# Optimization experiments

Hardware: AMD Instinct MI355X
Metric: run time of the kernel (lower is better)

The kernel has to match this reference:

```python
import jax, jax.numpy as jnp
import numpy as np

GROUPS = 32
EPS = 1e-6


def group_norm(x, gamma, beta):
    # x: [b, c, d, h, w]
    b, c, d, h, w = x.shape
    xg = x.reshape(b, GROUPS, c // GROUPS, d, h, w)
    mean = xg.mean(axis=(2, 3, 4, 5), keepdims=True)
    var = xg.var(axis=(2, 3, 4, 5), keepdims=True)
    xn = ((xg - mean) * jax.lax.rsqrt(var + EPS)).reshape(b, c, d, h, w)
    return xn * gamma[None, :, None, None, None] + beta[None, :, None, None, None]


def conv1x1(x, w, bias):
    # 1x1x1 Conv3d == channel matmul. x: [b,c,d,h,w], w: [out,in]
    return jnp.einsum('bcdhw,oc->bodhw', x, w) + bias[None, :, None, None, None]


def setup_inputs() -> dict:
    key = jax.random.key(0)
    ks = jax.random.split(key, 6)
    C = 256
    x = jax.random.normal(ks[0], (4, C, 16, 16, 16), dtype=jnp.float32)
    s = 1.0 / np.sqrt(C)
    return {
        'x': x,
        'gn_gamma': jnp.ones((C,), jnp.float32),
        'gn_beta': jnp.zeros((C,), jnp.float32),
        'wq': jax.random.normal(ks[1], (C, C), jnp.float32) * s,
        'bq': jnp.zeros((C,), jnp.float32),
        'wk': jax.random.normal(ks[2], (C, C), jnp.float32) * s,
        'bk': jnp.zeros((C,), jnp.float32),
        'wv': jax.random.normal(ks[3], (C, C), jnp.float32) * s,
        'bv': jnp.zeros((C,), jnp.float32),
        'wo': jax.random.normal(ks[4], (C, C), jnp.float32) * s,
        'bo': jnp.zeros((C,), jnp.float32),
    }


def reference(x, gn_gamma, gn_beta, wq, bq, wk, bk, wv, bv, wo, bo):
    b, c, d, h, w = x.shape
    n = d * h * w
    hn = group_norm(x, gn_gamma, gn_beta)
    q = conv1x1(hn, wq, bq).reshape(b, c, n)  # [b,c,n]
    k = conv1x1(hn, wk, bk).reshape(b, c, n)
    v = conv1x1(hn, wv, bv).reshape(b, c, n)
    # NOTE: no 1/sqrt(c) scaling, faithful to source
    scores = jnp.einsum('bci,bcj->bij', q, k)          # [b,n,n]
    attn = jax.nn.softmax(scores, axis=-1)
    out = jnp.einsum('bij,bcj->bci', attn, v)           # [b,c,n]
    out = out.reshape(b, c, d, h, w)
    out = conv1x1(out, wo, bo)
    return x + out
```

## Files before the change

### kernel.cpp

```cpp
#include <hip/hip_runtime.h>
#include <hip/hip_bf16.h>

#define C_ 256
#define N_ 4096
#define B_ 4
#define NG_ 32
#define CPG_ 8
#define SPLITS 2
#define JT_PER (N_ / 32 / SPLITS)

typedef _Float16 f16;
typedef __attribute__((ext_vector_type(8))) _Float16 f16v8;
typedef __attribute__((ext_vector_type(2))) __fp16 fp16v2;
typedef __attribute__((ext_vector_type(4))) float f32x4;

__device__ __forceinline__ f16v8 ldh(const f16* p) {
    return *reinterpret_cast<const f16v8*>(p);
}
__device__ __forceinline__ f32x4 mfma16(f16v8 a, f16v8 b, f32x4 c) {
    return __builtin_amdgcn_mfma_f32_16x16x32_f16(a, b, c, 0, 0, 0);
}
__device__ __forceinline__ unsigned int pkh(float a, float b) {
    fp16v2 t = __builtin_amdgcn_cvt_pkrtz(a, b);
    return __builtin_bit_cast(unsigned int, t);
}

__global__ __launch_bounds__(256) void conv_w_kernel(
    const float* __restrict__ wq, const float* __restrict__ wk,
    const float* __restrict__ wv, const float* __restrict__ wo,
    f16* __restrict__ wq16, f16* __restrict__ wk16,
    f16* __restrict__ wv16, f16* __restrict__ wo16)
{
    int idx = blockIdx.x * 256 + threadIdx.x;
    wq16[idx] = (f16)wq[idx];
    wk16[idx] = (f16)wk[idx];
    wv16[idx] = (f16)wv[idx];
    wo16[idx] = (f16)wo[idx];
}

__global__ __launch_bounds__(256) void gn_kernel(
    const float* __restrict__ x, const float* __restrict__ gamma,
    const float* __restrict__ beta, f16* __restrict__ hn)
{
    int b = blockIdx.x >> 5, g = blockIdx.x & 31;
    const float* xp = x + (size_t)(b * C_ + g * CPG_) * N_;
    int tid = threadIdx.x;
    float s = 0.f, s2 = 0.f;
    for (int idx = tid; idx < CPG_ * N_; idx += 256) {
        float v = xp[idx];
        s += v; s2 += v * v;
    }
    #pragma unroll
    for (int off = 32; off > 0; off >>= 1) {
        s  += __shfl_down(s, off);
        s2 += __shfl_down(s2, off);
    }
    __shared__ float rs[4], rs2[4], stat[2];
    if ((tid & 63) == 0) { rs[tid >> 6] = s; rs2[tid >> 6] = s2; }
    __syncthreads();
    if (tid == 0) {
        float S  = rs[0] + rs[1] + rs[2] + rs[3];
        float S2 = rs2[0] + rs2[1] + rs2[2] + rs2[3];
        float mean = S / (float)(CPG_ * N_);
        float var  = S2 / (float)(CPG_ * N_) - mean * mean;
        stat[0] = mean;
        stat[1] = rsqrtf(var + 1e-6f);
    }
    __syncthreads();
    float mean = stat[0], rstd = stat[1];
    float ga[CPG_], be[CPG_];
    #pragma unroll
    for (int cc = 0; cc < CPG_; cc++) {
        ga[cc] = gamma[g * CPG_ + cc] * rstd;
        be[cc] = beta[g * CPG_ + cc];
    }
    for (int i = tid; i < N_; i += 256) {
        f16v8 H;
        #pragma unroll
        for (int cc = 0; cc < CPG_; cc++)
            H[cc] = (f16)((xp[(size_t)cc * N_ + i] - mean) * ga[cc] + be[cc]);
        *reinterpret_cast<f16v8*>(hn + (size_t)(b * N_ + i) * C_ + g * CPG_) = H;
    }
}

__global__ __launch_bounds__(256) void proj_qk_kernel(
    const f16* __restrict__ hn, const f16* __restrict__ wq16,
    const f16* __restrict__ wk16, const float* __restrict__ bq,
    const float* __restrict__ bk, f16* __restrict__ qo, f16* __restrict__ ko)
{
    int it = blockIdx.x, b = blockIdx.y, which = blockIdx.z;
    const f16* wgt = which ? wk16 : wq16;
    const float* bias = which ? bk : bq;
    f16* outp = which ? ko : qo;
    int tid = threadIdx.x, w = tid >> 6, l = tid & 63;
    int l15 = l & 15, lhi = l >> 4;
    int i0 = it * 64 + w * 16;
    size_t arow = (size_t)(b * N_ + i0 + l15) * C_ + lhi * 8;
    f16v8 af[8];
    #pragma unroll
    for (int kk = 0; kk < 8; kk++) af[kk] = ldh(hn + arow + kk * 32);
    for (int oc = 0; oc < 16; oc++) {
        f32x4 acc = {0.f, 0.f, 0.f, 0.f};
        size_t wrow = (size_t)(oc * 16 + l15) * C_ + lhi * 8;
        #pragma unroll
        for (int kk = 0; kk < 8; kk++)
            acc = mfma16(af[kk], ldh(wgt + wrow + kk * 32), acc);
        float bia = bias[oc * 16 + l15];
        #pragma unroll
        for (int r = 0; r < 4; r++)
            outp[(size_t)(b * N_ + i0 + lhi * 4 + r) * C_ + oc * 16 + l15] =
                (f16)(acc[r] + bia);
    }
}

__global__ __launch_bounds__(256) void proj_v_kernel(
    const f16* __restrict__ hn, const f16* __restrict__ wv16,
    const float* __restrict__ bv, f16* __restrict__ vT)
{
    int it = blockIdx.x, b = blockIdx.y;
    int tid = threadIdx.x, w = tid >> 6, l = tid & 63;
    int l15 = l & 15, lhi = l >> 4;
    int o0 = w * 64, i0 = it * 64;
    f32x4 acc[4][4];
    #pragma unroll
    for (int mc = 0; mc < 4; mc++)
        #pragma unroll
        for (int nc = 0; nc < 4; nc++) acc[mc][nc] = (f32x4){0.f, 0.f, 0.f, 0.f};
    for (int kk = 0; kk < 8; kk++) {
        f16v8 af[4], bfv[4];
        #pragma unroll
        for (int mc = 0; mc < 4; mc++)
            af[mc] = ldh(wv16 + (size_t)(o0 + mc * 16 + l15) * C_ + kk * 32 + lhi * 8);
        #pragma unroll
        for (int nc = 0; nc < 4; nc++)
            bfv[nc] = ldh(hn + (size_t)(b * N_ + i0 + nc * 16 + l15) * C_ + kk * 32 + lhi * 8);
        #pragma unroll
        for (int mc = 0; mc < 4; mc++)
            #pragma unroll
            for (int nc = 0; nc < 4; nc++)
                acc[mc][nc] = mfma16(af[mc], bfv[nc], acc[mc][nc]);
    }
    #pragma unroll
    for (int mc = 0; mc < 4; mc++) {
        float bia[4];
        #pragma unroll
        for (int r = 0; r < 4; r++) bia[r] = bv[o0 + mc * 16 + lhi * 4 + r];
        #pragma unroll
        for (int nc = 0; nc < 4; nc++)
            #pragma unroll
            for (int r = 0; r < 4; r++) {
                int o = o0 + mc * 16 + lhi * 4 + r;
                int i = i0 + nc * 16 + l15;
                vT[(size_t)(b * C_ + o) * N_ + i] = (f16)(acc[mc][nc][r] + bia[r]);
            }
    }
}

__device__ __forceinline__ void stage_k(const f16* kbase, f16* dst, int j0,
                                        int w, int l) {
    #pragma unroll
    for (int rd = 0; rd < 4; rd++) {
        int cb = (rd * 4 + w) * 64;
        int mc = cb + l;
        int row = mc >> 5;
        int xoff = ((mc & 31) << 4) ^ ((row & 7) << 4);
        const f16* gsrc = kbase + (size_t)(j0 + row) * C_ + (xoff >> 1);
        __builtin_amdgcn_global_load_lds(
            (const __attribute__((address_space(1))) void*)gsrc,
            (__attribute__((address_space(3))) void*)(dst + (size_t)cb * 8),
            16, 0, 0);
    }
}
__device__ __forceinline__ void stage_v(const f16* vbase, f16* dst, int j0,
                                        int w, int l) {
    int tid = w * 64 + l;
    int colu = ((l & 3) ^ ((l >> 3) & 3)) * 8;
    #pragma unroll
    for (int s = 0; s < 4; s++) {
        int cb = s * 256 + w * 64;
        const f16* gsrc = vbase + (size_t)(s * 64 + (tid >> 2)) * N_ + j0 + colu;
        __builtin_amdgcn_global_load_lds(
            (const __attribute__((address_space(1))) void*)gsrc,
            (__attribute__((address_space(3))) void*)(dst + (size_t)cb * 8),
            16, 0, 0);
    }
}

__global__ __launch_bounds__(256, 2) void flash_split_kernel(
    const f16* __restrict__ q, const f16* __restrict__ k,
    const f16* __restrict__ vT,
    f16* __restrict__ o0p, f16* __restrict__ o1p,
    float2* __restrict__ stats)
{
    int bi = blockIdx.x;
    int g = bi & 7;
    int it = bi >> 3;
    int b = g >> 1, split = g & 1;
    int tid = threadIdx.x, w = tid >> 6, l = tid & 63;
    int l15 = l & 15, lhi = l >> 4;
    int i0 = it * 64 + w * 16;
    int jt0 = split * JT_PER;
    __shared__ __align__(16) f16 kb[2][32][256];
    __shared__ __align__(16) f16 vb[2][256][32];
    __shared__ __align__(16) unsigned int Plds[4][16][20];

    const f16* kbase = k + (size_t)b * N_ * C_;
    const f16* vbase = vT + (size_t)b * C_ * N_;

    f16v8 qf[8];
    size_t qrow = (size_t)(b * N_ + i0 + l15) * C_ + lhi * 8;
    #pragma unroll
    for (int kk = 0; kk < 8; kk++) qf[kk] = ldh(q + qrow + kk * 32);

    f32x4 oacc[16];
    #pragma unroll
    for (int cc = 0; cc < 16; cc++) oacc[cc] = (f32x4){0.f, 0.f, 0.f, 0.f};
    float m = -1e30f, rsum = 0.f;

    int lhiV = lhi ^ ((l15 >> 1) & 3);

    stage_k(kbase, &kb[0][0][0], jt0 * 32, w, l);
    stage_v(vbase, &vb[0][0][0], jt0 * 32, w, l);
    __syncthreads();

    for (int jt = 0; jt < JT_PER; jt++) {
        int cur = jt & 1;
        int j0 = (jt0 + jt) * 32;

        if (jt + 1 < JT_PER) {
            stage_k(kbase, &kb[cur ^ 1][0][0], j0 + 32, w, l);
            stage_v(vbase, &vb[cur ^ 1][0][0], j0 + 32, w, l);
        }

        const char* kbc = (const char*)&kb[cur][0][0];
        f32x4 s0 = {0.f, 0.f, 0.f, 0.f};
        f32x4 s1 = {0.f, 0.f, 0.f, 0.f};
        #pragma unroll
        for (int kk = 0; kk < 8; kk++) {
            {
                int row = l15;
                int off = row * 512 + ((kk * 64 + lhi * 16) ^ ((row & 7) << 4));
                f16v8 kf = *reinterpret_cast<const f16v8*>(kbc + off);
                s0 = mfma16(kf, qf[kk], s0);
            }
            {
                int row = 16 + l15;
                int off = row * 512 + ((kk * 64 + lhi * 16) ^ ((row & 7) << 4));
                f16v8 kf = *reinterpret_cast<const f16v8*>(kbc + off);
                s1 = mfma16(kf, qf[kk], s1);
            }
        }

        float mt = fmaxf(fmaxf(fmaxf(s0[0], s0[1]), fmaxf(s0[2], s0[3])),
                         fmaxf(fmaxf(s1[0], s1[1]), fmaxf(s1[2], s1[3])));
        mt = fmaxf(mt, __shfl_xor(mt, 16));
        mt = fmaxf(mt, __shfl_xor(mt, 32));
        if (!__all(mt <= m + 8.f)) {
            float mn = fmaxf(m, mt);
            float sc = __expf(m - mn);
            m = mn;
            rsum *= sc;
            #pragma unroll
            for (int cc = 0; cc < 16; cc++) {
                #pragma unroll
                for (int r = 0; r < 4; r++) oacc[cc][r] *= sc;
            }
        }
        float p0[4], p1[4];
        float ls = 0.f;
        #pragma unroll
        for (int r = 0; r < 4; r++) {
            p0[r] = __expf(s0[r] - m);
            p1[r] = __expf(s1[r] - m);
            ls += p0[r] + p1[r];
        }
        rsum += ls;

        uint2 pa = {pkh(p0[0], p0[1]), pkh(p0[2], p0[3])};
        uint2 pb = {pkh(p1[0], p1[1]), pkh(p1[2], p1[3])};
        *reinterpret_cast<uint2*>(&Plds[w][l15][lhi * 2])     = pa;
        *reinterpret_cast<uint2*>(&Plds[w][l15][8 + lhi * 2]) = pb;
        f16v8 pfB = *reinterpret_cast<const f16v8*>(&Plds[w][l15][lhi * 4]);

        const f16* vbc = &vb[cur][0][0];
        #pragma unroll
        for (int cc = 0; cc < 16; cc++) {
            f16v8 vf = ldh(vbc + (cc * 16 + l15) * 32 + lhiV * 8);
            oacc[cc] = mfma16(vf, pfB, oacc[cc]);
        }

        __syncthreads();
    }

    rsum += __shfl_xor(rsum, 16);
    rsum += __shfl_xor(rsum, 32);
    float inv = 1.f / rsum;

    f16* op = split ? o1p : o0p;
    size_t obase = (size_t)(b * N_ + i0 + l15) * C_;
    #pragma unroll
    for (int cc = 0; cc < 16; cc++) {
        uint2 st = {pkh(oacc[cc][0] * inv, oacc[cc][1] * inv),
                    pkh(oacc[cc][2] * inv, oacc[cc][3] * inv)};
        *reinterpret_cast<uint2*>(op + obase + cc * 16 + lhi * 4) = st;
    }
    if (lhi == 0)
        stats[((size_t)split * B_ + b) * N_ + i0 + l15] = make_float2(m, rsum);
}

__global__ __launch_bounds__(256) void final_kernel(
    const f16* __restrict__ o0p, const f16* __restrict__ o1p,
    const float2* __restrict__ stats, const f16* __restrict__ wo16,
    const float* __restrict__ bo, const float* __restrict__ x,
    float* __restrict__ out)
{
    int it = blockIdx.x, b = blockIdx.y;
    int tid = threadIdx.x, w = tid >> 6, l = tid & 63;
    int l15 = l & 15, lhi = l >> 4;
    int o0 = w * 64, i0 = it * 64;

    f16 w0h[4], w1h[4];
    #pragma unroll
    for (int nc = 0; nc < 4; nc++) {
        int row = i0 + nc * 16 + l15;
        float2 s0 = stats[(size_t)b * N_ + row];
        float2 s1 = stats[((size_t)B_ + b) * N_ + row];
        float M = fmaxf(s0.x, s1.x);
        float a0 = s0.y * __expf(s0.x - M);
        float a1 = s1.y * __expf(s1.x - M);
        float inv = 1.f / (a0 + a1);
        w0h[nc] = (f16)(a0 * inv);
        w1h[nc] = (f16)(a1 * inv);
    }

    f32x4 acc[4][4];
    #pragma unroll
    for (int mc = 0; mc < 4; mc++)
        #pragma unroll
        for (int nc = 0; nc < 4; nc++) acc[mc][nc] = (f32x4){0.f, 0.f, 0.f, 0.f};
    for (int kk = 0; kk < 8; kk++) {
        f16v8 af[4], bfv[4];
        #pragma unroll
        for (int mc = 0; mc < 4; mc++)
            af[mc] = ldh(wo16 + (size_t)(o0 + mc * 16 + l15) * C_ + kk * 32 + lhi * 8);
        #pragma unroll
        for (int nc = 0; nc < 4; nc++) {
            size_t off = (size_t)(b * N_ + i0 + nc * 16 + l15) * C_ + kk * 32 + lhi * 8;
            f16v8 a = ldh(o0p + off);
            f16v8 c = ldh(o1p + off);
            bfv[nc] = a * w0h[nc] + c * w1h[nc];
        }
        #pragma unroll
        for (int mc = 0; mc < 4; mc++)
            #pragma unroll
            for (int nc = 0; nc < 4; nc++)
                acc[mc][nc] = mfma16(af[mc], bfv[nc], acc[mc][nc]);
    }
    #pragma unroll
    for (int mc = 0; mc < 4; mc++) {
        float bia[4];
        #pragma unroll
        for (int r = 0; r < 4; r++) bia[r] = bo[o0 + mc * 16 + lhi * 4 + r];
        #pragma unroll
        for (int nc = 0; nc < 4; nc++)
            #pragma unroll
            for (int r = 0; r < 4; r++) {
                int o = o0 + mc * 16 + lhi * 4 + r;
                int i = i0 + nc * 16 + l15;
                size_t idx = (size_t)(b * C_ + o) * N_ + i;
                out[idx] = x[idx] + acc[mc][nc][r] + bia[r];
            }
    }
}

extern "C" void kernel_launch(void* const* d_in, const int* in_sizes, int n_in,
                              void* d_out, int out_size, void* d_ws, size_t ws_size,
                              hipStream_t stream) {
    const float* x  = (const float*)d_in[0];
    const float* gg = (const float*)d_in[1];
    const float* gb = (const float*)d_in[2];
    const float* wq = (const float*)d_in[3];
    const float* bq = (const float*)d_in[4];
    const float* wk = (const float*)d_in[5];
    const float* bk = (const float*)d_in[6];
    const float* wv = (const float*)d_in[7];
    const float* bv = (const float*)d_in[8];
    const float* wo = (const float*)d_in[9];
    const float* bo = (const float*)d_in[10];
    float* out = (float*)d_out;

    char* p = (char*)d_ws;
    const size_t WSZ = (size_t)C_ * C_ * 2;
    const size_t HSZ = (size_t)B_ * N_ * C_ * 2;
    f16* wq16 = (f16*)p; p += WSZ;
    f16* wk16 = (f16*)p; p += WSZ;
    f16* wv16 = (f16*)p; p += WSZ;
    f16* wo16 = (f16*)p; p += WSZ;
    f16* hn   = (f16*)p; p += HSZ;
    f16* qo   = (f16*)p; p += HSZ;
    f16* ko   = (f16*)p; p += HSZ;
    f16* vt   = (f16*)p; p += HSZ;
    f16* o1p  = (f16*)p; p += HSZ;
    float2* stats = (float2*)p; p += (size_t)SPLITS * B_ * N_ * sizeof(float2);

    f16* o0p = hn;

    conv_w_kernel<<<dim3(C_ * C_ / 256), 256, 0, stream>>>(
        wq, wk, wv, wo, wq16, wk16, wv16, wo16);
    gn_kernel<<<dim3(B_ * NG_), 256, 0, stream>>>(x, gg, gb, hn);
    proj_qk_kernel<<<dim3(N_ / 64, B_, 2), 256, 0, stream>>>(
        hn, wq16, wk16, bq, bk, qo, ko);
    proj_v_kernel<<<dim3(N_ / 64, B_), 256, 0, stream>>>(hn, wv16, bv, vt);
    flash_split_kernel<<<dim3(N_ / 64 * B_ * SPLITS), 256, 0, stream>>>(
        qo, ko, vt, o0p, o1p, stats);
    final_kernel<<<dim3(N_ / 64, B_), 256, 0, stream>>>(
        o0p, o1p, stats, wo16, bo, x, out);
}
```

Before: 217.9 us.

## Process two query tiles per wave and split KV into four parts

```diff
diff --git a/kernel.cpp b/kernel.cpp
--- a/kernel.cpp
+++ b/kernel.cpp
@@ -6,7 +6,7 @@
 #define B_ 4
 #define NG_ 32
 #define CPG_ 8
-#define SPLITS 2
+#define SPLITS 4
 #define JT_PER (N_ / 32 / SPLITS)
 
 typedef _Float16 f16;
@@ -190,32 +190,43 @@
     const f16* __restrict__ q, const f16* __restrict__ k,
     const f16* __restrict__ vT,
     f16* __restrict__ o0p, f16* __restrict__ o1p,
+    f16* __restrict__ o2p, f16* __restrict__ o3p,
     float2* __restrict__ stats)
 {
     int bi = blockIdx.x;
-    int g = bi & 7;
-    int it = bi >> 3;
-    int b = g >> 1, split = g & 1;
+    int g = bi & 15;
+    int it = bi >> 4;
+    int b = g >> 2, split = g & 3;
     int tid = threadIdx.x, w = tid >> 6, l = tid & 63;
     int l15 = l & 15, lhi = l >> 4;
-    int i0 = it * 64 + w * 16;
+    int i0 = it * 128 + w * 32;
     int jt0 = split * JT_PER;
     __shared__ __align__(16) f16 kb[2][32][256];
     __shared__ __align__(16) f16 vb[2][256][32];
-    __shared__ __align__(16) unsigned int Plds[4][16][20];
+    __shared__ __align__(16) unsigned int Plds[4][2][16][20];
 
     const f16* kbase = k + (size_t)b * N_ * C_;
     const f16* vbase = vT + (size_t)b * C_ * N_;
 
-    f16v8 qf[8];
-    size_t qrow = (size_t)(b * N_ + i0 + l15) * C_ + lhi * 8;
-    #pragma unroll
-    for (int kk = 0; kk < 8; kk++) qf[kk] = ldh(q + qrow + kk * 32);
-
-    f32x4 oacc[16];
-    #pragma unroll
-    for (int cc = 0; cc < 16; cc++) oacc[cc] = (f32x4){0.f, 0.f, 0.f, 0.f};
-    float m = -1e30f, rsum = 0.f;
+    f16v8 qfA[8], qfB_[8];
+    {
+        size_t qrow0 = (size_t)(b * N_ + i0 + l15) * C_ + lhi * 8;
+        size_t qrow1 = (size_t)(b * N_ + i0 + 16 + l15) * C_ + lhi * 8;
+        #pragma unroll
+        for (int kk = 0; kk < 8; kk++) {
+            qfA[kk]  = ldh(q + qrow0 + kk * 32);
+            qfB_[kk] = ldh(q + qrow1 + kk * 32);
+        }
+    }
+
+    f32x4 oaccA[16], oaccB[16];
+    #pragma unroll
+    for (int cc = 0; cc < 16; cc++) {
+        oaccA[cc] = (f32x4){0.f, 0.f, 0.f, 0.f};
+        oaccB[cc] = (f32x4){0.f, 0.f, 0.f, 0.f};
+    }
+    float mA = -1e30f, rsA = 0.f;
+    float mB = -1e30f, rsB = 0.f;
 
     int lhiV = lhi ^ ((l15 >> 1) & 3);
 
@@ -233,83 +244,105 @@
         }
 
         const char* kbc = (const char*)&kb[cur][0][0];
-        f32x4 s0 = {0.f, 0.f, 0.f, 0.f};
-        f32x4 s1 = {0.f, 0.f, 0.f, 0.f};
+        f32x4 sA0 = {0.f,0.f,0.f,0.f}, sA1 = {0.f,0.f,0.f,0.f};
+        f32x4 sB0 = {0.f,0.f,0.f,0.f}, sB1 = {0.f,0.f,0.f,0.f};
         #pragma unroll
         for (int kk = 0; kk < 8; kk++) {
-            {
-                int row = l15;
-                int off = row * 512 + ((kk * 64 + lhi * 16) ^ ((row & 7) << 4));
-                f16v8 kf = *reinterpret_cast<const f16v8*>(kbc + off);
-                s0 = mfma16(kf, qf[kk], s0);
-            }
-            {
-                int row = 16 + l15;
-                int off = row * 512 + ((kk * 64 + lhi * 16) ^ ((row & 7) << 4));
-                f16v8 kf = *reinterpret_cast<const f16v8*>(kbc + off);
-                s1 = mfma16(kf, qf[kk], s1);
-            }
-        }
-
-        float mt = fmaxf(fmaxf(fmaxf(s0[0], s0[1]), fmaxf(s0[2], s0[3])),
-                         fmaxf(fmaxf(s1[0], s1[1]), fmaxf(s1[2], s1[3])));
-        mt = fmaxf(mt, __shfl_xor(mt, 16));
-        mt = fmaxf(mt, __shfl_xor(mt, 32));
-        if (!__all(mt <= m + 8.f)) {
-            float mn = fmaxf(m, mt);
-            float sc = __expf(m - mn);
-            m = mn;
-            rsum *= sc;
+            int row0 = l15, row1 = 16 + l15;
+            int off0 = row0 * 512 + ((kk * 64 + lhi * 16) ^ ((row0 & 7) << 4));
+            int off1 = row1 * 512 + ((kk * 64 + lhi * 16) ^ ((row1 & 7) << 4));
+            f16v8 kf0 = *reinterpret_cast<const f16v8*>(kbc + off0);
+            f16v8 kf1 = *reinterpret_cast<const f16v8*>(kbc + off1);
+            sA0 = mfma16(kf0, qfA[kk], sA0);
+            sA1 = mfma16(kf1, qfA[kk], sA1);
+            sB0 = mfma16(kf0, qfB_[kk], sB0);
+            sB1 = mfma16(kf1, qfB_[kk], sB1);
+        }
+
+        float mtA = fmaxf(fmaxf(fmaxf(sA0[0], sA0[1]), fmaxf(sA0[2], sA0[3])),
+                          fmaxf(fmaxf(sA1[0], sA1[1]), fmaxf(sA1[2], sA1[3])));
+        float mtB = fmaxf(fmaxf(fmaxf(sB0[0], sB0[1]), fmaxf(sB0[2], sB0[3])),
+                          fmaxf(fmaxf(sB1[0], sB1[1]), fmaxf(sB1[2], sB1[3])));
+        mtA = fmaxf(mtA, __shfl_xor(mtA, 16));
+        mtA = fmaxf(mtA, __shfl_xor(mtA, 32));
+        mtB = fmaxf(mtB, __shfl_xor(mtB, 16));
+        mtB = fmaxf(mtB, __shfl_xor(mtB, 32));
+        if (!__all(mtA <= mA + 8.f && mtB <= mB + 8.f)) {
+            float mnA = fmaxf(mA, mtA), mnB = fmaxf(mB, mtB);
+            float scA = __expf(mA - mnA), scB = __expf(mB - mnB);
+            mA = mnA; mB = mnB;
+            rsA *= scA; rsB *= scB;
             #pragma unroll
             for (int cc = 0; cc < 16; cc++) {
                 #pragma unroll
-                for (int r = 0; r < 4; r++) oacc[cc][r] *= sc;
+                for (int r = 0; r < 4; r++) {
+                    oaccA[cc][r] *= scA;
+                    oaccB[cc][r] *= scB;
+                }
             }
         }
-        float p0[4], p1[4];
-        float ls = 0.f;
+        float pA0[4], pA1[4], pB0[4], pB1[4];
+        float lsA = 0.f, lsB = 0.f;
         #pragma unroll
         for (int r = 0; r < 4; r++) {
-            p0[r] = __expf(s0[r] - m);
-            p1[r] = __expf(s1[r] - m);
-            ls += p0[r] + p1[r];
-        }
-        rsum += ls;
-
-        uint2 pa = {pkh(p0[0], p0[1]), pkh(p0[2], p0[3])};
-        uint2 pb = {pkh(p1[0], p1[1]), pkh(p1[2], p1[3])};
-        *reinterpret_cast<uint2*>(&Plds[w][l15][lhi * 2])     = pa;
-        *reinterpret_cast<uint2*>(&Plds[w][l15][8 + lhi * 2]) = pb;
-        f16v8 pfB = *reinterpret_cast<const f16v8*>(&Plds[w][l15][lhi * 4]);
+            pA0[r] = __expf(sA0[r] - mA);
+            pA1[r] = __expf(sA1[r] - mA);
+            pB0[r] = __expf(sB0[r] - mB);
+            pB1[r] = __expf(sB1[r] - mB);
+            lsA += pA0[r] + pA1[r];
+            lsB += pB0[r] + pB1[r];
+        }
+        rsA += lsA; rsB += lsB;
+
+        {
+            uint2 pa = {pkh(pA0[0], pA0[1]), pkh(pA0[2], pA0[3])};
+            uint2 pb = {pkh(pA1[0], pA1[1]), pkh(pA1[2], pA1[3])};
+            *reinterpret_cast<uint2*>(&Plds[w][0][l15][lhi * 2])     = pa;
+            *reinterpret_cast<uint2*>(&Plds[w][0][l15][8 + lhi * 2]) = pb;
+            uint2 pc = {pkh(pB0[0], pB0[1]), pkh(pB0[2], pB0[3])};
+            uint2 pd = {pkh(pB1[0], pB1[1]), pkh(pB1[2], pB1[3])};
+            *reinterpret_cast<uint2*>(&Plds[w][1][l15][lhi * 2])     = pc;
+            *reinterpret_cast<uint2*>(&Plds[w][1][l15][8 + lhi * 2]) = pd;
+        }
+        f16v8 pfA = *reinterpret_cast<const f16v8*>(&Plds[w][0][l15][lhi * 4]);
+        f16v8 pfB = *reinterpret_cast<const f16v8*>(&Plds[w][1][l15][lhi * 4]);
 
         const f16* vbc = &vb[cur][0][0];
         #pragma unroll
         for (int cc = 0; cc < 16; cc++) {
             f16v8 vf = ldh(vbc + (cc * 16 + l15) * 32 + lhiV * 8);
-            oacc[cc] = mfma16(vf, pfB, oacc[cc]);
+            oaccA[cc] = mfma16(vf, pfA, oaccA[cc]);
+            oaccB[cc] = mfma16(vf, pfB, oaccB[cc]);
         }
 
         __syncthreads();
     }
 
-    rsum += __shfl_xor(rsum, 16);
-    rsum += __shfl_xor(rsum, 32);
-    float inv = 1.f / rsum;
-
-    f16* op = split ? o1p : o0p;
-    size_t obase = (size_t)(b * N_ + i0 + l15) * C_;
+    rsA += __shfl_xor(rsA, 16); rsA += __shfl_xor(rsA, 32);
+    rsB += __shfl_xor(rsB, 16); rsB += __shfl_xor(rsB, 32);
+    float invA = 1.f / rsA, invB = 1.f / rsB;
+
+    f16* op = (split == 0) ? o0p : (split == 1) ? o1p : (split == 2) ? o2p : o3p;
+    size_t obaseA = (size_t)(b * N_ + i0 + l15) * C_;
+    size_t obaseB = (size_t)(b * N_ + i0 + 16 + l15) * C_;
     #pragma unroll
     for (int cc = 0; cc < 16; cc++) {
-        uint2 st = {pkh(oacc[cc][0] * inv, oacc[cc][1] * inv),
-                    pkh(oacc[cc][2] * inv, oacc[cc][3] * inv)};
-        *reinterpret_cast<uint2*>(op + obase + cc * 16 + lhi * 4) = st;
-    }
-    if (lhi == 0)
-        stats[((size_t)split * B_ + b) * N_ + i0 + l15] = make_float2(m, rsum);
+        uint2 stA = {pkh(oaccA[cc][0] * invA, oaccA[cc][1] * invA),
+                     pkh(oaccA[cc][2] * invA, oaccA[cc][3] * invA)};
+        uint2 stB = {pkh(oaccB[cc][0] * invB, oaccB[cc][1] * invB),
+                     pkh(oaccB[cc][2] * invB, oaccB[cc][3] * invB)};
+        *reinterpret_cast<uint2*>(op + obaseA + cc * 16 + lhi * 4) = stA;
+        *reinterpret_cast<uint2*>(op + obaseB + cc * 16 + lhi * 4) = stB;
+    }
+    if (lhi == 0) {
+        stats[((size_t)split * B_ + b) * N_ + i0 + l15]      = make_float2(mA, rsA);
+        stats[((size_t)split * B_ + b) * N_ + i0 + 16 + l15] = make_float2(mB, rsB);
+    }
 }
 
 __global__ __launch_bounds__(256) void final_kernel(
     const f16* __restrict__ o0p, const f16* __restrict__ o1p,
+    const f16* __restrict__ o2p, const f16* __restrict__ o3p,
     const float2* __restrict__ stats, const f16* __restrict__ wo16,
     const float* __restrict__ bo, const float* __restrict__ x,
     float* __restrict__ out)
@@ -319,18 +352,26 @@
     int l15 = l & 15, lhi = l >> 4;
     int o0 = w * 64, i0 = it * 64;
 
-    f16 w0h[4], w1h[4];
+    f16 wh[4][SPLITS];
     #pragma unroll
     for (int nc = 0; nc < 4; nc++) {
         int row = i0 + nc * 16 + l15;
-        float2 s0 = stats[(size_t)b * N_ + row];
-        float2 s1 = stats[((size_t)B_ + b) * N_ + row];
-        float M = fmaxf(s0.x, s1.x);
-        float a0 = s0.y * __expf(s0.x - M);
-        float a1 = s1.y * __expf(s1.x - M);
-        float inv = 1.f / (a0 + a1);
-        w0h[nc] = (f16)(a0 * inv);
-        w1h[nc] = (f16)(a1 * inv);
+        float2 st[SPLITS];
+        float M = -1e30f;
+        #pragma unroll
+        for (int s = 0; s < SPLITS; s++) {
+            st[s] = stats[((size_t)s * B_ + b) * N_ + row];
+            M = fmaxf(M, st[s].x);
+        }
+        float a[SPLITS], L = 0.f;
+        #pragma unroll
+        for (int s = 0; s < SPLITS; s++) {
+            a[s] = st[s].y * __expf(st[s].x - M);
+            L += a[s];
+        }
+        float inv = 1.f / L;
+        #pragma unroll
+        for (int s = 0; s < SPLITS; s++) wh[nc][s] = (f16)(a[s] * inv);
     }
 
     f32x4 acc[4][4];
@@ -346,9 +387,11 @@
         #pragma unroll
         for (int nc = 0; nc < 4; nc++) {
             size_t off = (size_t)(b * N_ + i0 + nc * 16 + l15) * C_ + kk * 32 + lhi * 8;
-            f16v8 a = ldh(o0p + off);
-            f16v8 c = ldh(o1p + off);
-            bfv[nc] = a * w0h[nc] + c * w1h[nc];
+            f16v8 v0 = ldh(o0p + off);
+            f16v8 v1 = ldh(o1p + off);
+            f16v8 v2 = ldh(o2p + off);
+            f16v8 v3 = ldh(o3p + off);
+            bfv[nc] = v0 * wh[nc][0] + v1 * wh[nc][1] + v2 * wh[nc][2] + v3 * wh[nc][3];
         }
         #pragma unroll
         for (int mc = 0; mc < 4; mc++)
@@ -392,6 +435,7 @@
     char* p = (char*)d_ws;
     const size_t WSZ = (size_t)C_ * C_ * 2;
     const size_t HSZ = (size_t)B_ * N_ * C_ * 2;
+    const size_t HN  = (size_t)B_ * N_ * C_;
     f16* wq16 = (f16*)p; p += WSZ;
     f16* wk16 = (f16*)p; p += WSZ;
     f16* wv16 = (f16*)p; p += WSZ;
@@ -400,10 +444,13 @@
     f16* qo   = (f16*)p; p += HSZ;
     f16* ko   = (f16*)p; p += HSZ;
     f16* vt   = (f16*)p; p += HSZ;
-    f16* o1p  = (f16*)p; p += HSZ;
+    f16* oex  = (f16*)p; p += 3 * HSZ;
     float2* stats = (float2*)p; p += (size_t)SPLITS * B_ * N_ * sizeof(float2);
 
     f16* o0p = hn;
+    f16* o1p = oex;
+    f16* o2p = oex + HN;
+    f16* o3p = oex + 2 * HN;
 
     conv_w_kernel<<<dim3(C_ * C_ / 256), 256, 0, stream>>>(
         wq, wk, wv, wo, wq16, wk16, wv16, wo16);
@@ -411,8 +458,8 @@
     proj_qk_kernel<<<dim3(N_ / 64, B_, 2), 256, 0, stream>>>(
         hn, wq16, wk16, bq, bk, qo, ko);
     proj_v_kernel<<<dim3(N_ / 64, B_), 256, 0, stream>>>(hn, wv16, bv, vt);
-    flash_split_kernel<<<dim3(N_ / 64 * B_ * SPLITS), 256, 0, stream>>>(
-        qo, ko, vt, o0p, o1p, stats);
+    flash_split_kernel<<<dim3(N_ / 128 * B_ * SPLITS), 256, 0, stream>>>(
+        qo, ko, vt, o0p, o1p, o2p, o3p, stats);
     final_kernel<<<dim3(N_ / 64, B_), 256, 0, stream>>>(
-        o0p, o1p, stats, wo16, bo, x, out);
-}
+        o0p, o1p, o2p, o3p, stats, wo16, bo, x, out);
+}
```

New measurement: 228.8 us. 5.0% more time.
